# Kernel tuning notes

Hardware: AMD Instinct MI355X
Metric: run time of the kernel (lower is better)

## Reference

```python
import jax, jax.numpy as jnp
import numpy as np

B_SZ, N_IN, N_CTX, UNITS, RANK = 4096, 4096, 512, 4096, 256


def setup_inputs() -> dict:
    key = jax.random.key(0)
    ks = jax.random.split(key, 8)
    inputs = jax.random.normal(ks[0], (B_SZ, N_IN), dtype=jnp.float32)
    context = jax.random.normal(ks[1], (B_SZ, N_CTX), dtype=jnp.float32)
    # Orthogonal-ish init approximated by scaled normals (math-equivalent shapes)
    U = jax.random.normal(ks[2], (N_IN, RANK), dtype=jnp.float32) / np.sqrt(N_IN)
    S = jax.random.uniform(ks[3], (RANK,), dtype=jnp.float32, minval=0.5, maxval=1.5)
    V = jax.random.normal(ks[4], (UNITS, RANK), dtype=jnp.float32) / np.sqrt(UNITS)
    W = jax.random.normal(ks[5], (N_CTX, RANK), dtype=jnp.float32) / np.sqrt(N_CTX)
    B = jnp.zeros((RANK,), dtype=jnp.float32)
    bias = jnp.zeros((UNITS,), dtype=jnp.float32)
    return {"inputs": inputs, "context": context, "U": U, "S": S, "V": V, "W": W, "B": B, "bias": bias}


def reference(inputs, context, U, S, V, W, B, bias):
    # chi[b,r] = sigmoid(context @ W + B)
    chi = jax.nn.sigmoid(context @ W + B)                  # [B, R]
    # Original: kernel[b,n,m] = sum_r U[n,r]*S[r]*chi[b,r]*V[m,r];
    # out[b,m] = sum_n x[b,n]*kernel[b,n,m]. Algebraically equal to:
    t = (inputs @ U) * (S * chi)                           # [B, R]
    out = t @ V.T + bias                                   # first '+ self.bias'
    out = out + bias                                       # 'outputs += self.bias' (use_bias=True)
    return jax.nn.relu(out)
```

## Files before the change

### kernel.cpp

```cpp
#include <hip/hip_runtime.h>

#define B_SZ 4096
#define N_IN 4096
#define N_CTX 512
#define UNITS 4096
#define RANK 256
#define ZSPLIT 8

typedef __attribute__((ext_vector_type(8))) __bf16 bf16x8;
typedef __attribute__((ext_vector_type(4))) float f32x4;
typedef __attribute__((ext_vector_type(8))) unsigned short ushort8;
typedef __attribute__((ext_vector_type(4))) unsigned short ushort4v;

__device__ __forceinline__ unsigned short f2bf(float f) {
    unsigned int u = __float_as_uint(f);
    u += 0x7FFFu + ((u >> 16) & 1u);
    return (unsigned short)(u >> 16);
}
__device__ __forceinline__ float bf2f(unsigned short h) {
    return __uint_as_float(((unsigned int)h) << 16);
}
__device__ __forceinline__ void gload_lds16(const unsigned short* g, unsigned short* l) {
    __builtin_amdgcn_global_load_lds(
        (const __attribute__((address_space(1))) unsigned int*)g,
        (__attribute__((address_space(3))) unsigned int*)l, 16, 0, 0);
}
__device__ __forceinline__ bf16x8 ldfrag(const unsigned short* p) {
    ushort8 t = *(const ushort8*)p;
    return __builtin_bit_cast(bf16x8, t);
}

__global__ void transpose_cvt(const float* __restrict__ src, unsigned short* __restrict__ dst,
                              int R, int C) {
    __shared__ unsigned short t[64][66];
    int rb = blockIdx.x * 64, cb = blockIdx.y * 64;
    int tid = threadIdx.x;
    int r = tid >> 4, c4 = (tid & 15) * 4;
    for (int i = 0; i < 4; i++) {
        float4 v = *(const float4*)(src + (size_t)(rb + r + i * 16) * C + cb + c4);
        t[r + i * 16][c4 + 0] = f2bf(v.x);
        t[r + i * 16][c4 + 1] = f2bf(v.y);
        t[r + i * 16][c4 + 2] = f2bf(v.z);
        t[r + i * 16][c4 + 3] = f2bf(v.w);
    }
    __syncthreads();
    int c = tid >> 3, r8 = (tid & 7) * 8;
    for (int j = 0; j < 2; j++) {
        int cc = c + j * 32;
        ushort8 o;
        for (int k = 0; k < 8; k++) o[k] = t[r8 + k][cc];
        *(ushort8*)(dst + (size_t)(cb + cc) * R + rb + r8) = o;
    }
}

__global__ void conv_kernel(const float* __restrict__ src, unsigned short* __restrict__ dst) {
    int i = blockIdx.x * 256 + threadIdx.x;
    float4 v = ((const float4*)src)[i];
    ushort4v r = { f2bf(v.x), f2bf(v.y), f2bf(v.z), f2bf(v.w) };
    ((ushort4v*)dst)[i] = r;
}

__launch_bounds__(256, 4)
__global__ void k1_chi(const float* __restrict__ ctx, const unsigned short* __restrict__ WT,
                       const float* __restrict__ S, const float* __restrict__ Bb,
                       unsigned short* __restrict__ Schi) {
    __shared__ unsigned short As[32 * 64];
    __shared__ unsigned short Bs[64 * 64];
    int tid = threadIdx.x, w = tid >> 6, lane = tid & 63;
    int ln15 = lane & 15, quad = lane >> 4;
    int wr = w >> 1, wc = w & 1;
    int tm = blockIdx.y * 32, tn = blockIdx.x * 64;
    f32x4 acc2[2] = {};
    int arow = tid >> 3, ac4 = (tid & 7) * 4;
    const float* ag = ctx + (size_t)(tm + arow) * N_CTX + ac4;
    int brow0 = w * 16, bl8 = lane >> 3, bk8 = (lane & 7) * 8;
    for (int kt = 0; kt < 8; kt++) {
        int k0 = kt * 64;
        for (int c = 0; c < 2; c++) {
            int row = brow0 + c * 8 + bl8;
            gload_lds16(WT + (size_t)(tn + row) * N_CTX + k0 + bk8, Bs + row * 64 + bk8);
        }
        for (int i = 0; i < 2; i++) {
            float4 v = *(const float4*)(ag + k0 + i * 32);
            ushort4v a4 = { f2bf(v.x), f2bf(v.y), f2bf(v.z), f2bf(v.w) };
            *(ushort4v*)(As + arow * 64 + ac4 + i * 32) = a4;
        }
        __syncthreads();
        for (int kh = 0; kh < 2; kh++) {
            bf16x8 af = ldfrag(As + (wr * 16 + ln15) * 64 + kh * 32 + quad * 8);
            for (int j = 0; j < 2; j++) {
                bf16x8 bfr = ldfrag(Bs + (wc * 32 + j * 16 + ln15) * 64 + kh * 32 + quad * 8);
                acc2[j] = __builtin_amdgcn_mfma_f32_16x16x32_bf16(af, bfr, acc2[j], 0, 0, 0);
            }
        }
        __syncthreads();
    }
    for (int j = 0; j < 2; j++) {
        int col = tn + wc * 32 + j * 16 + ln15;
        float sv = S[col], bv = Bb[col];
        for (int r = 0; r < 4; r++) {
            int row = tm + wr * 16 + quad * 4 + r;
            float x = acc2[j][r] + bv;
            float chi = sv / (1.f + __expf(-x));
            Schi[(size_t)row * RANK + col] = f2bf(chi);
        }
    }
}

__launch_bounds__(256, 4)
__global__ void k2_t0(const float* __restrict__ X, const unsigned short* __restrict__ UT,
                      unsigned short* __restrict__ T0p) {
    __shared__ unsigned short As[64 * 64];
    __shared__ unsigned short Bs[128 * 64];
    int tid = threadIdx.x, w = tid >> 6, lane = tid & 63;
    int ln15 = lane & 15, quad = lane >> 4;
    int wr = w >> 1, wc = w & 1;
    int tm = blockIdx.y * 64, tn = blockIdx.x * 128;
    int kbase = blockIdx.z * (N_IN / ZSPLIT);
    f32x4 acc[2][4] = {};
    int arow = tid >> 2, ac4 = (tid & 3) * 4;
    const float* ag = X + (size_t)(tm + arow) * N_IN + kbase + ac4;
    int brow0 = w * 32, bl8 = lane >> 3, bk8 = (lane & 7) * 8;
    for (int kt = 0; kt < (N_IN / ZSPLIT) / 64; kt++) {
        int k0 = kt * 64;
        for (int c = 0; c < 4; c++) {
            int row = brow0 + c * 8 + bl8;
            gload_lds16(UT + (size_t)(tn + row) * N_IN + kbase + k0 + bk8, Bs + row * 64 + bk8);
        }
        for (int i = 0; i < 4; i++) {
            float4 v = *(const float4*)(ag + k0 + i * 16);
            ushort4v a4 = { f2bf(v.x), f2bf(v.y), f2bf(v.z), f2bf(v.w) };
            *(ushort4v*)(As + arow * 64 + ac4 + i * 16) = a4;
        }
        __syncthreads();
        for (int kh = 0; kh < 2; kh++) {
            bf16x8 af[2], bfr[4];
            for (int i = 0; i < 2; i++)
                af[i] = ldfrag(As + (wr * 32 + i * 16 + ln15) * 64 + kh * 32 + quad * 8);
            for (int j = 0; j < 4; j++)
                bfr[j] = ldfrag(Bs + (wc * 64 + j * 16 + ln15) * 64 + kh * 32 + quad * 8);
            for (int i = 0; i < 2; i++)
                for (int j = 0; j < 4; j++)
                    acc[i][j] = __builtin_amdgcn_mfma_f32_16x16x32_bf16(af[i], bfr[j], acc[i][j], 0, 0, 0);
        }
        __syncthreads();
    }
    unsigned short* P = T0p + (size_t)blockIdx.z * B_SZ * RANK;
    for (int i = 0; i < 2; i++)
        for (int j = 0; j < 4; j++) {
            int col = tn + wc * 64 + j * 16 + ln15;
            for (int r = 0; r < 4; r++) {
                int row = tm + wr * 32 + i * 16 + quad * 4 + r;
                P[(size_t)row * RANK + col] = f2bf(acc[i][j][r]);
            }
        }
}

__global__ void e_red(const unsigned short* __restrict__ T0p, const unsigned short* __restrict__ Schi,
                      unsigned short* __restrict__ T) {
    int i = blockIdx.x * 256 + threadIdx.x;
    const size_t stride = (size_t)B_SZ * RANK;
    float a[8] = {};
    for (int z = 0; z < ZSPLIT; z++) {
        ushort8 p = *(const ushort8*)(T0p + z * stride + (size_t)i * 8);
        for (int k = 0; k < 8; k++) a[k] += bf2f(p[k]);
    }
    ushort8 s = *(const ushort8*)(Schi + (size_t)i * 8);
    ushort8 o;
    for (int k = 0; k < 8; k++) o[k] = f2bf(a[k] * bf2f(s[k]));
    *(ushort8*)(T + (size_t)i * 8) = o;
}

__launch_bounds__(256, 3)
__global__ void k3_out(const unsigned short* __restrict__ T, const unsigned short* __restrict__ Vb,
                       const float* __restrict__ bias, float* __restrict__ out) {
    __shared__ unsigned short As[128 * 64];
    __shared__ unsigned short Bs[128 * 64];
    int tid = threadIdx.x, w = tid >> 6, lane = tid & 63;
    int ln15 = lane & 15, quad = lane >> 4;
    int wr = w >> 1, wc = w & 1;
    int tn = blockIdx.x * 128, tm = blockIdx.y * 128;
    f32x4 acc[4][4] = {};
    int row0 = w * 32, bl8 = lane >> 3, bk8 = (lane & 7) * 8;
    for (int kt = 0; kt < RANK / 64; kt++) {
        int k0 = kt * 64;
        for (int c = 0; c < 4; c++) {
            int row = row0 + c * 8 + bl8;
            gload_lds16(T  + (size_t)(tm + row) * RANK + k0 + bk8, As + row * 64 + bk8);
            gload_lds16(Vb + (size_t)(tn + row) * RANK + k0 + bk8, Bs + row * 64 + bk8);
        }
        __syncthreads();
        for (int kh = 0; kh < 2; kh++) {
            bf16x8 af[4], bfr[4];
            for (int i = 0; i < 4; i++)
                af[i] = ldfrag(As + (wr * 64 + i * 16 + ln15) * 64 + kh * 32 + quad * 8);
            for (int j = 0; j < 4; j++)
                bfr[j] = ldfrag(Bs + (wc * 64 + j * 16 + ln15) * 64 + kh * 32 + quad * 8);
            for (int i = 0; i < 4; i++)
                for (int j = 0; j < 4; j++)
                    acc[i][j] = __builtin_amdgcn_mfma_f32_16x16x32_bf16(af[i], bfr[j], acc[i][j], 0, 0, 0);
        }
        __syncthreads();
    }
    for (int j = 0; j < 4; j++) {
        int col = tn + wc * 64 + j * 16 + ln15;
        float bv = 2.f * bias[col];
        for (int i = 0; i < 4; i++)
            for (int r = 0; r < 4; r++) {
                int row = tm + wr * 64 + i * 16 + quad * 4 + r;
                float v = acc[i][j][r] + bv;
                out[(size_t)row * UNITS + col] = fmaxf(v, 0.f);
            }
    }
}

extern "C" void kernel_launch(void* const* d_in, const int* in_sizes, int n_in,
                              void* d_out, int out_size, void* d_ws, size_t ws_size,
                              hipStream_t stream) {
    (void)in_sizes; (void)n_in; (void)out_size; (void)ws_size;
    const float* inputs  = (const float*)d_in[0];
    const float* context = (const float*)d_in[1];
    const float* U       = (const float*)d_in[2];
    const float* S       = (const float*)d_in[3];
    const float* V       = (const float*)d_in[4];
    const float* W       = (const float*)d_in[5];
    const float* Bb      = (const float*)d_in[6];
    const float* bias    = (const float*)d_in[7];
    float* out = (float*)d_out;

    char* ws = (char*)d_ws;
    size_t o = 0;
    unsigned short* UT   = (unsigned short*)(ws + o); o += (size_t)RANK * N_IN * 2;
    unsigned short* WT   = (unsigned short*)(ws + o); o += (size_t)RANK * N_CTX * 2;
    unsigned short* Vb   = (unsigned short*)(ws + o); o += (size_t)UNITS * RANK * 2;
    unsigned short* Schi = (unsigned short*)(ws + o); o += (size_t)B_SZ * RANK * 2;
    unsigned short* T    = (unsigned short*)(ws + o); o += (size_t)B_SZ * RANK * 2;
    unsigned short* T0p  = (unsigned short*)(ws + o); o += (size_t)ZSPLIT * B_SZ * RANK * 2;

    transpose_cvt<<<dim3(N_IN / 64, RANK / 64), 256, 0, stream>>>(U, UT, N_IN, RANK);
    transpose_cvt<<<dim3(N_CTX / 64, RANK / 64), 256, 0, stream>>>(W, WT, N_CTX, RANK);
    conv_kernel<<<(UNITS * RANK) / (256 * 4), 256, 0, stream>>>(V, Vb);

    k2_t0<<<dim3(RANK / 128, B_SZ / 64, ZSPLIT), 256, 0, stream>>>(inputs, UT, T0p);
    k1_chi<<<dim3(RANK / 64, B_SZ / 32), 256, 0, stream>>>(context, WT, S, Bb, Schi);
    e_red<<<(B_SZ * RANK) / (256 * 8), 256, 0, stream>>>(T0p, Schi, T);
    k3_out<<<dim3(UNITS / 128, B_SZ / 128), 256, 0, stream>>>(T, Vb, bias, out);
}
```

Measured before the change: 185.6 us.

## XOR-swizzle LDS tiles, merge weight prep kernels, shrink k3 M-tile

Adds an XOR swizzle to the LDS layout of the A and B tiles in all three GEMM kernels, so that MFMA fragment reads avoid bank conflicts. The A loads become 8-wide bf16 stores. The three weight-conversion kernels (U and W transposes, V conversion) are merged into one prep launch of 800 blocks, which saves two launches. The output GEMM tile drops from 128x128 to 64x128 with occupancy raised to 4, giving more blocks and less LDS per block, at the cost of less reuse of each V tile.

```diff
diff --git a/kernel.cpp b/kernel.cpp
--- a/kernel.cpp
+++ b/kernel.cpp
@@ -30,35 +30,42 @@
     return __builtin_bit_cast(bf16x8, t);
 }
 
-__global__ void transpose_cvt(const float* __restrict__ src, unsigned short* __restrict__ dst,
-                              int R, int C) {
+__global__ void prep(const float* __restrict__ U, const float* __restrict__ W,
+                     const float* __restrict__ V,
+                     unsigned short* __restrict__ UT, unsigned short* __restrict__ WT,
+                     unsigned short* __restrict__ Vb) {
     __shared__ unsigned short t[64][66];
-    int rb = blockIdx.x * 64, cb = blockIdx.y * 64;
-    int tid = threadIdx.x;
-    int r = tid >> 4, c4 = (tid & 15) * 4;
-    for (int i = 0; i < 4; i++) {
-        float4 v = *(const float4*)(src + (size_t)(rb + r + i * 16) * C + cb + c4);
-        t[r + i * 16][c4 + 0] = f2bf(v.x);
-        t[r + i * 16][c4 + 1] = f2bf(v.y);
-        t[r + i * 16][c4 + 2] = f2bf(v.z);
-        t[r + i * 16][c4 + 3] = f2bf(v.w);
-    }
-    __syncthreads();
-    int c = tid >> 3, r8 = (tid & 7) * 8;
-    for (int j = 0; j < 2; j++) {
-        int cc = c + j * 32;
-        ushort8 o;
-        for (int k = 0; k < 8; k++) o[k] = t[r8 + k][cc];
-        *(ushort8*)(dst + (size_t)(cb + cc) * R + rb + r8) = o;
-    }
-}
-
-__global__ void conv_kernel(const float* __restrict__ src, unsigned short* __restrict__ dst) {
-    int i = blockIdx.x * 256 + threadIdx.x;
-    float4 v = ((const float4*)src)[i];
-    ushort4v r = { f2bf(v.x), f2bf(v.y), f2bf(v.z), f2bf(v.w) };
-    ((ushort4v*)dst)[i] = r;
-}
+    int bid = blockIdx.x, tid = threadIdx.x;
+    if (bid < 288) {
+        const float* src; unsigned short* dst; int R, C, rb, cb;
+        if (bid < 256) { src = U; dst = UT; R = N_IN; C = RANK; rb = (bid & 63) * 64; cb = (bid >> 6) * 64; }
+        else { int b = bid - 256; src = W; dst = WT; R = N_CTX; C = RANK; rb = (b & 7) * 64; cb = (b >> 3) * 64; }
+        int r = tid >> 4, c4 = (tid & 15) * 4;
+        for (int i = 0; i < 4; i++) {
+            float4 v = *(const float4*)(src + (size_t)(rb + r + i * 16) * C + cb + c4);
+            t[r + i * 16][c4 + 0] = f2bf(v.x);
+            t[r + i * 16][c4 + 1] = f2bf(v.y);
+            t[r + i * 16][c4 + 2] = f2bf(v.z);
+            t[r + i * 16][c4 + 3] = f2bf(v.w);
+        }
+        __syncthreads();
+        int c = tid >> 3, r8 = (tid & 7) * 8;
+        for (int j = 0; j < 2; j++) {
+            int cc = c + j * 32;
+            ushort8 o;
+            for (int k = 0; k < 8; k++) o[k] = t[r8 + k][cc];
+            *(ushort8*)(dst + (size_t)(cb + cc) * R + rb + r8) = o;
+        }
+    } else {
+        size_t base = (size_t)(bid - 288) * 2048 + (size_t)tid * 8;
+        float4 a = *(const float4*)(V + base);
+        float4 b = *(const float4*)(V + base + 4);
+        ushort8 o = { f2bf(a.x), f2bf(a.y), f2bf(a.z), f2bf(a.w),
+                      f2bf(b.x), f2bf(b.y), f2bf(b.z), f2bf(b.w) };
+        *(ushort8*)(Vb + base) = o;
+    }
+}
+
 
 __launch_bounds__(256, 4)
 __global__ void k1_chi(const float* __restrict__ ctx, const unsigned short* __restrict__ WT,
@@ -71,25 +78,31 @@
     int wr = w >> 1, wc = w & 1;
     int tm = blockIdx.y * 32, tn = blockIdx.x * 64;
     f32x4 acc2[2] = {};
-    int arow = tid >> 3, ac4 = (tid & 7) * 4;
-    const float* ag = ctx + (size_t)(tm + arow) * N_CTX + ac4;
-    int brow0 = w * 16, bl8 = lane >> 3, bk8 = (lane & 7) * 8;
+    int arow = tid >> 3, acs = tid & 7;
+    const float* ag = ctx + (size_t)(tm + arow) * N_CTX + acs * 8;
+    unsigned short* al = As + arow * 64 + (acs ^ (arow & 7)) * 8;
+    int bl8 = lane >> 3, bcs = lane & 7;
+    int bgc = (bcs ^ bl8) * 8;
     for (int kt = 0; kt < 8; kt++) {
         int k0 = kt * 64;
         for (int c = 0; c < 2; c++) {
-            int row = brow0 + c * 8 + bl8;
-            gload_lds16(WT + (size_t)(tn + row) * N_CTX + k0 + bk8, Bs + row * 64 + bk8);
-        }
-        for (int i = 0; i < 2; i++) {
-            float4 v = *(const float4*)(ag + k0 + i * 32);
-            ushort4v a4 = { f2bf(v.x), f2bf(v.y), f2bf(v.z), f2bf(v.w) };
-            *(ushort4v*)(As + arow * 64 + ac4 + i * 32) = a4;
+            int row = w * 16 + c * 8 + bl8;
+            gload_lds16(WT + (size_t)(tn + row) * N_CTX + k0 + bgc, Bs + row * 64 + bcs * 8);
+        }
+        {
+            float4 v0 = *(const float4*)(ag + k0);
+            float4 v1 = *(const float4*)(ag + k0 + 4);
+            ushort8 a8 = { f2bf(v0.x), f2bf(v0.y), f2bf(v0.z), f2bf(v0.w),
+                           f2bf(v1.x), f2bf(v1.y), f2bf(v1.z), f2bf(v1.w) };
+            *(ushort8*)al = a8;
         }
         __syncthreads();
         for (int kh = 0; kh < 2; kh++) {
-            bf16x8 af = ldfrag(As + (wr * 16 + ln15) * 64 + kh * 32 + quad * 8);
+            int ch = kh * 4 + quad;
+            bf16x8 af = ldfrag(As + (wr * 16 + ln15) * 64 + (ch ^ (ln15 & 7)) * 8);
             for (int j = 0; j < 2; j++) {
-                bf16x8 bfr = ldfrag(Bs + (wc * 32 + j * 16 + ln15) * 64 + kh * 32 + quad * 8);
+                int row = wc * 32 + j * 16 + ln15;
+                bf16x8 bfr = ldfrag(Bs + row * 64 + (ch ^ (ln15 & 7)) * 8);
                 acc2[j] = __builtin_amdgcn_mfma_f32_16x16x32_bf16(af, bfr, acc2[j], 0, 0, 0);
             }
         }
@@ -118,27 +131,39 @@
     int tm = blockIdx.y * 64, tn = blockIdx.x * 128;
     int kbase = blockIdx.z * (N_IN / ZSPLIT);
     f32x4 acc[2][4] = {};
-    int arow = tid >> 2, ac4 = (tid & 3) * 4;
-    const float* ag = X + (size_t)(tm + arow) * N_IN + kbase + ac4;
-    int brow0 = w * 32, bl8 = lane >> 3, bk8 = (lane & 7) * 8;
+    int arow = tid >> 2, acs0 = tid & 3;
+    const float* ag = X + (size_t)(tm + arow) * N_IN + kbase;
+    unsigned short* al0 = As + arow * 64 + ((acs0 + 0) ^ (arow & 7)) * 8;
+    unsigned short* al1 = As + arow * 64 + ((acs0 + 4) ^ (arow & 7)) * 8;
+    int bl8 = lane >> 3, bcs = lane & 7;
+    int bgc = (bcs ^ bl8) * 8;
     for (int kt = 0; kt < (N_IN / ZSPLIT) / 64; kt++) {
         int k0 = kt * 64;
         for (int c = 0; c < 4; c++) {
-            int row = brow0 + c * 8 + bl8;
-            gload_lds16(UT + (size_t)(tn + row) * N_IN + kbase + k0 + bk8, Bs + row * 64 + bk8);
-        }
-        for (int i = 0; i < 4; i++) {
-            float4 v = *(const float4*)(ag + k0 + i * 16);
-            ushort4v a4 = { f2bf(v.x), f2bf(v.y), f2bf(v.z), f2bf(v.w) };
-            *(ushort4v*)(As + arow * 64 + ac4 + i * 16) = a4;
+            int row = w * 32 + c * 8 + bl8;
+            gload_lds16(UT + (size_t)(tn + row) * N_IN + kbase + k0 + bgc, Bs + row * 64 + bcs * 8);
+        }
+        {
+            float4 v0 = *(const float4*)(ag + k0 + acs0 * 8);
+            float4 v1 = *(const float4*)(ag + k0 + acs0 * 8 + 4);
+            float4 u0 = *(const float4*)(ag + k0 + (acs0 + 4) * 8);
+            float4 u1 = *(const float4*)(ag + k0 + (acs0 + 4) * 8 + 4);
+            ushort8 a8 = { f2bf(v0.x), f2bf(v0.y), f2bf(v0.z), f2bf(v0.w),
+                           f2bf(v1.x), f2bf(v1.y), f2bf(v1.z), f2bf(v1.w) };
+            ushort8 b8 = { f2bf(u0.x), f2bf(u0.y), f2bf(u0.z), f2bf(u0.w),
+                           f2bf(u1.x), f2bf(u1.y), f2bf(u1.z), f2bf(u1.w) };
+            *(ushort8*)al0 = a8;
+            *(ushort8*)al1 = b8;
         }
         __syncthreads();
         for (int kh = 0; kh < 2; kh++) {
+            int ch = kh * 4 + quad;
+            int sw = (ch ^ (ln15 & 7)) * 8;
             bf16x8 af[2], bfr[4];
             for (int i = 0; i < 2; i++)
-                af[i] = ldfrag(As + (wr * 32 + i * 16 + ln15) * 64 + kh * 32 + quad * 8);
+                af[i] = ldfrag(As + (wr * 32 + i * 16 + ln15) * 64 + sw);
             for (int j = 0; j < 4; j++)
-                bfr[j] = ldfrag(Bs + (wc * 64 + j * 16 + ln15) * 64 + kh * 32 + quad * 8);
+                bfr[j] = ldfrag(Bs + (wc * 64 + j * 16 + ln15) * 64 + sw);
             for (int i = 0; i < 2; i++)
                 for (int j = 0; j < 4; j++)
                     acc[i][j] = __builtin_amdgcn_mfma_f32_16x16x32_bf16(af[i], bfr[j], acc[i][j], 0, 0, 0);
@@ -171,32 +196,38 @@
     *(ushort8*)(T + (size_t)i * 8) = o;
 }
 
-__launch_bounds__(256, 3)
+__launch_bounds__(256, 4)
 __global__ void k3_out(const unsigned short* __restrict__ T, const unsigned short* __restrict__ Vb,
                        const float* __restrict__ bias, float* __restrict__ out) {
-    __shared__ unsigned short As[128 * 64];
+    __shared__ unsigned short As[64 * 64];
     __shared__ unsigned short Bs[128 * 64];
     int tid = threadIdx.x, w = tid >> 6, lane = tid & 63;
     int ln15 = lane & 15, quad = lane >> 4;
     int wr = w >> 1, wc = w & 1;
-    int tn = blockIdx.x * 128, tm = blockIdx.y * 128;
-    f32x4 acc[4][4] = {};
-    int row0 = w * 32, bl8 = lane >> 3, bk8 = (lane & 7) * 8;
+    int tn = blockIdx.x * 128, tm = blockIdx.y * 64;
+    f32x4 acc[2][4] = {};
+    int bl8 = lane >> 3, bcs = lane & 7;
+    int bgc = (bcs ^ bl8) * 8;
     for (int kt = 0; kt < RANK / 64; kt++) {
         int k0 = kt * 64;
+        for (int c = 0; c < 2; c++) {
+            int row = w * 16 + c * 8 + bl8;
+            gload_lds16(T + (size_t)(tm + row) * RANK + k0 + bgc, As + row * 64 + bcs * 8);
+        }
         for (int c = 0; c < 4; c++) {
-            int row = row0 + c * 8 + bl8;
-            gload_lds16(T  + (size_t)(tm + row) * RANK + k0 + bk8, As + row * 64 + bk8);
-            gload_lds16(Vb + (size_t)(tn + row) * RANK + k0 + bk8, Bs + row * 64 + bk8);
+            int row = w * 32 + c * 8 + bl8;
+            gload_lds16(Vb + (size_t)(tn + row) * RANK + k0 + bgc, Bs + row * 64 + bcs * 8);
         }
         __syncthreads();
         for (int kh = 0; kh < 2; kh++) {
-            bf16x8 af[4], bfr[4];
-            for (int i = 0; i < 4; i++)
-                af[i] = ldfrag(As + (wr * 64 + i * 16 + ln15) * 64 + kh * 32 + quad * 8);
+            int ch = kh * 4 + quad;
+            int sw = (ch ^ (ln15 & 7)) * 8;
+            bf16x8 af[2], bfr[4];
+            for (int i = 0; i < 2; i++)
+                af[i] = ldfrag(As + (wr * 32 + i * 16 + ln15) * 64 + sw);
             for (int j = 0; j < 4; j++)
-                bfr[j] = ldfrag(Bs + (wc * 64 + j * 16 + ln15) * 64 + kh * 32 + quad * 8);
-            for (int i = 0; i < 4; i++)
+                bfr[j] = ldfrag(Bs + (wc * 64 + j * 16 + ln15) * 64 + sw);
+            for (int i = 0; i < 2; i++)
                 for (int j = 0; j < 4; j++)
                     acc[i][j] = __builtin_amdgcn_mfma_f32_16x16x32_bf16(af[i], bfr[j], acc[i][j], 0, 0, 0);
         }
@@ -205,9 +236,9 @@
     for (int j = 0; j < 4; j++) {
         int col = tn + wc * 64 + j * 16 + ln15;
         float bv = 2.f * bias[col];
-        for (int i = 0; i < 4; i++)
+        for (int i = 0; i < 2; i++)
             for (int r = 0; r < 4; r++) {
-                int row = tm + wr * 64 + i * 16 + quad * 4 + r;
+                int row = tm + wr * 32 + i * 16 + quad * 4 + r;
                 float v = acc[i][j][r] + bv;
                 out[(size_t)row * UNITS + col] = fmaxf(v, 0.f);
             }
@@ -237,12 +268,9 @@
     unsigned short* T    = (unsigned short*)(ws + o); o += (size_t)B_SZ * RANK * 2;
     unsigned short* T0p  = (unsigned short*)(ws + o); o += (size_t)ZSPLIT * B_SZ * RANK * 2;
 
-    transpose_cvt<<<dim3(N_IN / 64, RANK / 64), 256, 0, stream>>>(U, UT, N_IN, RANK);
-    transpose_cvt<<<dim3(N_CTX / 64, RANK / 64), 256, 0, stream>>>(W, WT, N_CTX, RANK);
-    conv_kernel<<<(UNITS * RANK) / (256 * 4), 256, 0, stream>>>(V, Vb);
-
+    prep<<<800, 256, 0, stream>>>(U, W, V, UT, WT, Vb);
     k2_t0<<<dim3(RANK / 128, B_SZ / 64, ZSPLIT), 256, 0, stream>>>(inputs, UT, T0p);
     k1_chi<<<dim3(RANK / 64, B_SZ / 32), 256, 0, stream>>>(context, WT, S, Bb, Schi);
     e_red<<<(B_SZ * RANK) / (256 * 8), 256, 0, stream>>>(T0p, Schi, T);
-    k3_out<<<dim3(UNITS / 128, B_SZ / 128), 256, 0, stream>>>(T, Vb, bias, out);
-}
+    k3_out<<<dim3(UNITS / 128, B_SZ / 64), 256, 0, stream>>>(T, Vb, bias, out);
+}
```

After: 178.8 us. 1.04x faster.
